# Kernel tuning notes

Hardware: AMD Instinct MI355X
Metric: run time of the kernel (lower is better)

Reference implementation:

```python
import jax, jax.numpy as jnp
import numpy as np

K_TOP = 32
TEMPERATURE = 0.1
EPS = 1e-12  # torch F.normalize eps


def _l2_normalize(x):
    n = jnp.linalg.norm(x, axis=-1, keepdims=True)
    return x / jnp.maximum(n, EPS)


def setup_inputs() -> dict:
    key = jax.random.key(0)
    kq, kk, kv = jax.random.split(key, 3)
    B, T, d_k, d_v, N = 4, 512, 512, 512, 65536
    queries = jax.random.normal(kq, (B, T, d_k), dtype=jnp.float32)
    keys = jax.random.normal(kk, (N, d_k), dtype=jnp.float32)
    values = jax.random.normal(kv, (N, d_v), dtype=jnp.float32)
    return {"queries": queries, "keys": keys, "values": values}


def reference(queries, keys, values):
    B, T, d_k = queries.shape
    d_v = values.shape[1]
    flat_q = queries.reshape(B * T, d_k)
    qn = _l2_normalize(flat_q)           # [BT, d_k]
    kn = _l2_normalize(keys)             # [N, d_k]
    scores = qn @ kn.T                   # [BT, N] cosine similarities
    topk_scores, topk_idx = jax.lax.top_k(scores, K_TOP)  # [BT, K]
    attn = jax.nn.softmax(topk_scores / TEMPERATURE, axis=-1)  # [BT, K]
    retrieved = values[topk_idx]         # [BT, K, d_v]
    aggregated = jnp.einsum('nk,nkd->nd', attn, retrieved)  # [BT, d_v]
    return (aggregated.reshape(B, T, d_v),
            attn.reshape(B, T, K_TOP),
            topk_idx.reshape(B, T, K_TOP))
```

## Files before the change

### kernel.cpp

```cpp
#include <hip/hip_runtime.h>
#include <math.h>

#define M_ROWS 2048
#define N_KEYS 65536
#define DKK 512
#define DVV 512
#define KTOP 32
#define NSPLIT 32
#define NRANGE (N_KEYS / NSPLIT)
#define BM 128
#define BN 128
#define NTILES (NRANGE / BN)
#define KSTEPS (DKK / 32)
#define CAP 8

typedef _Float16 f16x8 __attribute__((ext_vector_type(8)));
typedef _Float16 f16x4v __attribute__((ext_vector_type(4)));
typedef float f32x4 __attribute__((ext_vector_type(4)));


__device__ __forceinline__ void split4(const float4 v, float inv,
                                       _Float16* ph, _Float16* pl) {
  f16x4v h, l;
  float y;
  y = v.x * inv; h[0] = (_Float16)y; l[0] = (_Float16)(y - (float)h[0]);
  y = v.y * inv; h[1] = (_Float16)y; l[1] = (_Float16)(y - (float)h[1]);
  y = v.z * inv; h[2] = (_Float16)y; l[2] = (_Float16)(y - (float)h[2]);
  y = v.w * inv; h[3] = (_Float16)y; l[3] = (_Float16)(y - (float)h[3]);
  *(f16x4v*)ph = h; *(f16x4v*)pl = l;
}

__global__ void __launch_bounds__(256) norm_split_kernel(
    const float* __restrict__ q, const float* __restrict__ keys,
    _Float16* __restrict__ Qh, _Float16* __restrict__ Ql,
    _Float16* __restrict__ Kh, _Float16* __restrict__ Kl) {
  const int gw = (blockIdx.x * 256 + threadIdx.x) >> 6;
  const int lane = threadIdx.x & 63;
  const float* row; _Float16 *oh, *ol;
  if (gw < M_ROWS) {
    row = q + (size_t)gw * DKK; oh = Qh + (size_t)gw * DKK; ol = Ql + (size_t)gw * DKK;
  } else {
    const int n = gw - M_ROWS;
    if (n >= N_KEYS) return;
    row = keys + (size_t)n * DKK; oh = Kh + (size_t)n * DKK; ol = Kl + (size_t)n * DKK;
  }
  const float4 a = ((const float4*)row)[lane];
  const float4 b = ((const float4*)row)[lane + 64];
  float s = a.x*a.x + a.y*a.y + a.z*a.z + a.w*a.w
          + b.x*b.x + b.y*b.y + b.z*b.z + b.w*b.w;
#pragma unroll
  for (int off = 32; off; off >>= 1) s += __shfl_xor(s, off);
  const float inv = 1.0f / fmaxf(sqrtf(s), 1e-12f);
  split4(a, inv, oh + lane * 4,       ol + lane * 4);
  split4(b, inv, oh + 256 + lane * 4, ol + 256 + lane * 4);
}

__device__ __forceinline__ void insert32(float* tS, int* tI, float s, int idx) {
  const float ms = tS[31]; const int mi_ = tI[31];
  if (s < ms || (s == ms && idx > mi_)) return;
  int p = 0;
  while (p < KTOP && (tS[p] > s || (tS[p] == s && tI[p] < idx))) ++p;
  for (int qq = KTOP - 1; qq > p; --qq) { tS[qq] = tS[qq-1]; tI[qq] = tI[qq-1]; }
  tS[p] = s; tI[p] = idx;
}

__global__ void __launch_bounds__(256, 2) gemm_topk_kernel(
    const _Float16* __restrict__ Qh, const _Float16* __restrict__ Ql,
    const _Float16* __restrict__ Kh, const _Float16* __restrict__ Kl,
    float* __restrict__ pscore, int* __restrict__ pidx) {
  __shared__ _Float16 stAh[BM*32], stAl[BM*32], stBh[BN*32], stBl[BN*32];
  __shared__ float topS[128*33];
  __shared__ int   topI[128*33];
  __shared__ float candS[128*9];
  __shared__ int   candI[128*9];
  __shared__ float mS[128];
  __shared__ int   cnt[128];
  __shared__ int   sOver;

  const int tid  = threadIdx.x;
  const int lane = tid & 63;
  const int w    = tid >> 6;
  const int wr   = w >> 1, wc = w & 1;
  const int cl   = lane & 15;
  const int g    = lane >> 4;
  const int g4   = g * 4;
  const int qbase  = blockIdx.x * BM;
  const int nbase0 = blockIdx.y * NRANGE;

  if (tid < 128) {
    mS[tid] = -INFINITY; cnt[tid] = 0;
#pragma unroll
    for (int j = 0; j < KTOP; ++j) { topS[tid*33+j] = -INFINITY; topI[tid*33+j] = 0x7fffffff; }
  }
  if (tid == 0) sOver = 0;
  __syncthreads();

  for (int ct = 0; ct < NTILES; ++ct) {
    const int n0 = nbase0 + ct * BN;
    f32x4 acc[4][4];
#pragma unroll
    for (int mi = 0; mi < 4; ++mi)
#pragma unroll
      for (int ni = 0; ni < 4; ++ni) acc[mi][ni] = (f32x4)0.0f;

    for (int ks = 0; ks < KSTEPS; ++ks) {
      const int kof = ks * 32;
      f16x8 ld[8];
#pragma unroll
      for (int p = 0; p < 2; ++p) {
        const int id = tid + p * 256;
        const int r = id >> 2, o = id & 3;
        const size_t ga = (size_t)(qbase + r) * DKK + kof + o * 8;
        const size_t gb = (size_t)(n0 + r) * DKK + kof + o * 8;
        ld[p*4+0] = *(const f16x8*)&Qh[ga];
        ld[p*4+1] = *(const f16x8*)&Ql[ga];
        ld[p*4+2] = *(const f16x8*)&Kh[gb];
        ld[p*4+3] = *(const f16x8*)&Kl[gb];
      }
      __syncthreads();
#pragma unroll
      for (int p = 0; p < 2; ++p) {
        const int id = tid + p * 256;
        const int r = id >> 2, o = id & 3;
        const int sw = r * 32 + 8 * (o ^ ((r >> 1) & 3));
        *(f16x8*)&stAh[sw] = ld[p*4+0];
        *(f16x8*)&stAl[sw] = ld[p*4+1];
        *(f16x8*)&stBh[sw] = ld[p*4+2];
        *(f16x8*)&stBl[sw] = ld[p*4+3];
      }
      __syncthreads();

      f16x8 Ah[4], Al[4], Bh[4], Bl[4];
#pragma unroll
      for (int mi = 0; mi < 4; ++mi) {
        const int r = wr * 64 + mi * 16 + cl;
        const int sw = r * 32 + 8 * (g ^ ((r >> 1) & 3));
        Ah[mi] = *(const f16x8*)&stAh[sw];
        Al[mi] = *(const f16x8*)&stAl[sw];
      }
#pragma unroll
      for (int ni = 0; ni < 4; ++ni) {
        const int c = wc * 64 + ni * 16 + cl;
        const int sw = c * 32 + 8 * (g ^ ((c >> 1) & 3));
        Bh[ni] = *(const f16x8*)&stBh[sw];
        Bl[ni] = *(const f16x8*)&stBl[sw];
      }
#pragma unroll
      for (int mi = 0; mi < 4; ++mi)
#pragma unroll
        for (int ni = 0; ni < 4; ++ni) {
          acc[mi][ni] = __builtin_amdgcn_mfma_f32_16x16x32_f16(Al[mi], Bl[ni], acc[mi][ni], 0, 0, 0);
          acc[mi][ni] = __builtin_amdgcn_mfma_f32_16x16x32_f16(Al[mi], Bh[ni], acc[mi][ni], 0, 0, 0);
          acc[mi][ni] = __builtin_amdgcn_mfma_f32_16x16x32_f16(Ah[mi], Bl[ni], acc[mi][ni], 0, 0, 0);
          acc[mi][ni] = __builtin_amdgcn_mfma_f32_16x16x32_f16(Ah[mi], Bh[ni], acc[mi][ni], 0, 0, 0);
        }
    }

    float m[4][4];
#pragma unroll
    for (int mi = 0; mi < 4; ++mi) {
      const f32x4 mv = *(const f32x4*)&mS[wr * 64 + mi * 16 + g4];
      m[mi][0] = mv[0]; m[mi][1] = mv[1]; m[mi][2] = mv[2]; m[mi][3] = mv[3];
    }
    unsigned long long pend = 0ull;
#pragma unroll
    for (int mi = 0; mi < 4; ++mi)
#pragma unroll
      for (int ni = 0; ni < 4; ++ni)
#pragma unroll
        for (int j = 0; j < 4; ++j)
          if (acc[mi][ni][j] >= m[mi][j])
            pend |= 1ull << (mi * 16 + ni * 4 + j);

    for (;;) {
      if (pend) {
#pragma unroll
        for (int mi = 0; mi < 4; ++mi)
#pragma unroll
          for (int ni = 0; ni < 4; ++ni)
#pragma unroll
            for (int j = 0; j < 4; ++j) {
              const int bit = mi * 16 + ni * 4 + j;
              if (pend & (1ull << bit)) {
                const int r = wr * 64 + mi * 16 + g4 + j;
                const int t = atomicAdd(&cnt[r], 1);
                if (t < CAP) {
                  candS[r * 9 + t] = acc[mi][ni][j];
                  candI[r * 9 + t] = n0 + wc * 64 + ni * 16 + cl;
                  pend &= ~(1ull << bit);
                }
              }
            }
      }
      __syncthreads();
      if (tid < 128) {
        int nc = cnt[tid];
        if (nc > CAP) { sOver = 1; nc = CAP; }
        float* tS = &topS[tid * 33];
        int*   tI = &topI[tid * 33];
        for (int e = 0; e < nc; ++e) insert32(tS, tI, candS[tid * 9 + e], candI[tid * 9 + e]);
        mS[tid] = tS[KTOP - 1];
        cnt[tid] = 0;
      }
      __syncthreads();
      const int over = sOver;
      __syncthreads();
      if (tid == 0) sOver = 0;
      if (!over) break;
#pragma unroll
      for (int mi = 0; mi < 4; ++mi) {
        const f32x4 mv = *(const f32x4*)&mS[wr * 64 + mi * 16 + g4];
        m[mi][0] = mv[0]; m[mi][1] = mv[1]; m[mi][2] = mv[2]; m[mi][3] = mv[3];
      }
      unsigned long long keep = 0ull;
#pragma unroll
      for (int mi = 0; mi < 4; ++mi)
#pragma unroll
        for (int ni = 0; ni < 4; ++ni)
#pragma unroll
          for (int j = 0; j < 4; ++j) {
            const int bit = mi * 16 + ni * 4 + j;
            if ((pend & (1ull << bit)) && acc[mi][ni][j] >= m[mi][j])
              keep |= 1ull << bit;
          }
      pend = keep;
    }
  }

  if (tid < 128) {
    const size_t base = ((size_t)(qbase + tid) * NSPLIT + blockIdx.y) * KTOP;
    for (int j = 0; j < KTOP; ++j) {
      pscore[base + j] = topS[tid * 33 + j];
      pidx[base + j]   = topI[tid * 33 + j];
    }
  }
}


#define QB 128
#define NB 128
#define KC 32
#define FNTILES (NRANGE / NB)
#define KCH (DKK / KC)
#define LDST 132

__global__ void __launch_bounds__(256) norm_kernel(
    const float* __restrict__ q, const float* __restrict__ keys,
    float* __restrict__ qn, float* __restrict__ kinv) {
  const int gw = (blockIdx.x * 256 + threadIdx.x) >> 6;
  const int lane = threadIdx.x & 63;
  if (gw < M_ROWS) {
    const float* row = q + (size_t)gw * DKK;
    float4 a = ((const float4*)row)[lane];
    float4 b = ((const float4*)row)[lane + 64];
    float s = a.x*a.x + a.y*a.y + a.z*a.z + a.w*a.w
            + b.x*b.x + b.y*b.y + b.z*b.z + b.w*b.w;
#pragma unroll
    for (int off = 32; off; off >>= 1) s += __shfl_xor(s, off);
    const float inv = 1.0f / fmaxf(sqrtf(s), 1e-12f);
    float* orow = qn + (size_t)gw * DKK;
    ((float4*)orow)[lane]      = make_float4(a.x*inv, a.y*inv, a.z*inv, a.w*inv);
    ((float4*)orow)[lane + 64] = make_float4(b.x*inv, b.y*inv, b.z*inv, b.w*inv);
  } else {
    const int n = gw - M_ROWS;
    if (n < N_KEYS) {
      const float* row = keys + (size_t)n * DKK;
      float4 a = ((const float4*)row)[lane];
      float4 b = ((const float4*)row)[lane + 64];
      float s = a.x*a.x + a.y*a.y + a.z*a.z + a.w*a.w
              + b.x*b.x + b.y*b.y + b.z*b.z + b.w*b.w;
#pragma unroll
      for (int off = 32; off; off >>= 1) s += __shfl_xor(s, off);
      if (lane == 0) kinv[n] = 1.0f / fmaxf(sqrtf(s), 1e-12f);
    }
  }
}

__device__ __forceinline__ void lds_wr_tile(float* dst, int k8, int r, float4 v, float scale) {
  dst[(k8 * 4 + 0) * LDST + r] = v.x * scale;
  dst[(k8 * 4 + 1) * LDST + r] = v.y * scale;
  dst[(k8 * 4 + 2) * LDST + r] = v.z * scale;
  dst[(k8 * 4 + 3) * LDST + r] = v.w * scale;
}

__global__ void __launch_bounds__(256, 1) score_topk_kernel(
    const float* __restrict__ qn, const float* __restrict__ keys,
    const float* __restrict__ kinv,
    float* __restrict__ pscore, int* __restrict__ pidx) {
  __shared__ float u[16896];
  __shared__ float topS[QB * KTOP];
  __shared__ int   topI[QB * KTOP];

  const int tid = threadIdx.x;
  const int tx = tid & 15, ty = tid >> 4;
  const int qbase = blockIdx.y * QB;
  const int nbase0 = blockIdx.x * NRANGE;

  for (int i = tid; i < QB * KTOP; i += 256) { topS[i] = -INFINITY; topI[i] = 0; }
  __syncthreads();

  for (int t = 0; t < FNTILES; ++t) {
    const int n0 = nbase0 + t * NB;
    float acc[8][8];
#pragma unroll
    for (int i = 0; i < 8; ++i)
#pragma unroll
      for (int j = 0; j < 8; ++j) acc[i][j] = 0.0f;

#pragma unroll
    for (int p = 0; p < 4; ++p) {
      const int id = tid + p * 256;
      const int r = id >> 3, k8 = id & 7;
      const float4 va = *(const float4*)&qn[(size_t)(qbase + r) * DKK + k8 * 4];
      const float4 vb = *(const float4*)&keys[(size_t)(n0 + r) * DKK + k8 * 4];
      const float kv = kinv[n0 + r];
      lds_wr_tile(u, k8, r, va, 1.0f);
      lds_wr_tile(u + 4224, k8, r, vb, kv);
    }
    __syncthreads();

    for (int kc = 0; kc < KCH; ++kc) {
      float4 pa[4], pb[4]; float pk[4];
      const bool pre = (kc + 1 < KCH);
      if (pre) {
#pragma unroll
        for (int p = 0; p < 4; ++p) {
          const int id = tid + p * 256;
          const int r = id >> 3, k8 = id & 7;
          pa[p] = *(const float4*)&qn[(size_t)(qbase + r) * DKK + (kc + 1) * KC + k8 * 4];
          pb[p] = *(const float4*)&keys[(size_t)(n0 + r) * DKK + (kc + 1) * KC + k8 * 4];
          pk[p] = kinv[n0 + r];
        }
      }
      const float* As = u + (kc & 1) * 8448;
      const float* Bs = As + 4224;
#pragma unroll 4
      for (int kk = 0; kk < KC; ++kk) {
        const float4 a0 = *(const float4*)&As[kk * LDST + ty * 4];
        const float4 a1 = *(const float4*)&As[kk * LDST + ty * 4 + 64];
        const float4 b0 = *(const float4*)&Bs[kk * LDST + tx * 4];
        const float4 b1 = *(const float4*)&Bs[kk * LDST + tx * 4 + 64];
        const float av[8] = {a0.x,a0.y,a0.z,a0.w,a1.x,a1.y,a1.z,a1.w};
        const float bv[8] = {b0.x,b0.y,b0.z,b0.w,b1.x,b1.y,b1.z,b1.w};
#pragma unroll
        for (int i = 0; i < 8; ++i)
#pragma unroll
          for (int j = 0; j < 8; ++j)
            acc[i][j] = fmaf(av[i], bv[j], acc[i][j]);
      }
      if (pre) {
        float* Ad = u + ((kc + 1) & 1) * 8448;
        float* Bd = Ad + 4224;
#pragma unroll
        for (int p = 0; p < 4; ++p) {
          const int id = tid + p * 256;
          const int r = id >> 3, k8 = id & 7;
          lds_wr_tile(Ad, k8, r, pa[p], 1.0f);
          lds_wr_tile(Bd, k8, r, pb[p], pk[p]);
        }
      }
      __syncthreads();
    }

#pragma unroll
    for (int ib = 0; ib < 2; ++ib)
#pragma unroll
      for (int i = 0; i < 4; ++i) {
        const int r = ty * 4 + i + ib * 64;
#pragma unroll
        for (int jb = 0; jb < 2; ++jb) {
          *(float4*)&u[r * LDST + tx * 4 + jb * 64] =
              make_float4(acc[ib*4+i][jb*4+0], acc[ib*4+i][jb*4+1],
                          acc[ib*4+i][jb*4+2], acc[ib*4+i][jb*4+3]);
        }
      }
    __syncthreads();

    if (tid < QB) {
      const int row = tid;
      float* tS = &topS[row * KTOP];
      int*   tI = &topI[row * KTOP];
      float mSv = tS[KTOP - 1]; int mIv = tI[KTOP - 1];
      for (int c4 = 0; c4 < NB / 4; ++c4) {
        const float4 v = *(const float4*)&u[row * LDST + c4 * 4];
#pragma unroll
        for (int wv = 0; wv < 4; ++wv) {
          const float s = (&v.x)[wv];
          const int idx = n0 + c4 * 4 + wv;
          if (s > mSv || (s == mSv && idx < mIv)) {
            int p = 0;
            while (p < KTOP && (tS[p] > s || (tS[p] == s && tI[p] < idx))) ++p;
            for (int qq = KTOP - 1; qq > p; --qq) { tS[qq] = tS[qq-1]; tI[qq] = tI[qq-1]; }
            tS[p] = s; tI[p] = idx;
            mSv = tS[KTOP - 1]; mIv = tI[KTOP - 1];
          }
        }
      }
    }
    __syncthreads();
  }

  if (tid < QB) {
    const size_t base = ((size_t)(qbase + tid) * NSPLIT + blockIdx.x) * KTOP;
    for (int j = 0; j < KTOP; ++j) {
      pscore[base + j] = topS[tid * KTOP + j];
      pidx[base + j]   = topI[tid * KTOP + j];
    }
  }
}

__global__ void __launch_bounds__(256) merge_kernel(
    const float* __restrict__ pscore, const int* __restrict__ pidx,
    const float* __restrict__ values,
    float* __restrict__ out_agg, float* __restrict__ out_attn, float* __restrict__ out_idx) {
  __shared__ float attn_s[KTOP];
  __shared__ int   sel_i[KTOP];
  const int row = blockIdx.x;
  const int tid = threadIdx.x;

  if (tid < 64) {
    const int lane = tid;
    const float* ps = pscore + (size_t)row * NSPLIT * KTOP;
    const int*   pi = pidx   + (size_t)row * NSPLIT * KTOP;
    int pos = 0;
    float s; int idx;
    if (lane < NSPLIT) { s = ps[lane * KTOP]; idx = pi[lane * KTOP]; }
    else { s = -INFINITY; idx = 0x7fffffff; }
    for (int it = 0; it < KTOP; ++it) {
      float wsv = s; int wi = idx; int wl = lane;
#pragma unroll
      for (int off = 32; off; off >>= 1) {
        const float os = __shfl_xor(wsv, off);
        const int   oi = __shfl_xor(wi, off);
        const int   ol = __shfl_xor(wl, off);
        if (os > wsv || (os == wsv && oi < wi)) { wsv = os; wi = oi; wl = ol; }
      }
      if (lane == 0) { attn_s[it] = wsv; sel_i[it] = wi; }
      if (lane == wl) {
        ++pos;
        if (pos < KTOP) { s = ps[lane * KTOP + pos]; idx = pi[lane * KTOP + pos]; }
        else { s = -INFINITY; idx = 0x7fffffff; }
      }
    }
  }
  __syncthreads();
  if (tid < KTOP) {
    const float mm = attn_s[0];
    const float e = expf((attn_s[tid] - mm) * 10.0f);
    float tsum = e;
#pragma unroll
    for (int off = 16; off; off >>= 1) tsum += __shfl_xor(tsum, off);
    const float a = e / tsum;
    out_attn[(size_t)row * KTOP + tid] = a;
    out_idx [(size_t)row * KTOP + tid] = (float)sel_i[tid];
    attn_s[tid] = a;
  }
  __syncthreads();

  const int d = tid * 2;
  float2 accv = make_float2(0.0f, 0.0f);
  for (int j = 0; j < KTOP; ++j) {
    const float wgt = attn_s[j];
    const float2 v = *(const float2*)&values[(size_t)sel_i[j] * DVV + d];
    accv.x = fmaf(wgt, v.x, accv.x);
    accv.y = fmaf(wgt, v.y, accv.y);
  }
  *(float2*)&out_agg[(size_t)row * DVV + d] = accv;
}

extern "C" void kernel_launch(void* const* d_in, const int* in_sizes, int n_in,
                              void* d_out, int out_size, void* d_ws, size_t ws_size,
                              hipStream_t stream) {
  const float* q      = (const float*)d_in[0];
  const float* keys   = (const float*)d_in[1];
  const float* values = (const float*)d_in[2];

  float* out      = (float*)d_out;
  float* out_agg  = out;
  float* out_attn = out + (size_t)M_ROWS * DVV;
  float* out_idx  = out_attn + (size_t)M_ROWS * KTOP;

  const size_t needFast =
      (size_t)M_ROWS * DKK * 2 * 2
    + (size_t)N_KEYS * DKK * 2 * 2
    + (size_t)M_ROWS * NSPLIT * KTOP * 8;

  if (ws_size >= needFast) {
    _Float16* Qh = (_Float16*)d_ws;
    _Float16* Ql = Qh + (size_t)M_ROWS * DKK;
    _Float16* Kh = Ql + (size_t)M_ROWS * DKK;
    _Float16* Kl = Kh + (size_t)N_KEYS * DKK;
    float* pscore = (float*)(Kl + (size_t)N_KEYS * DKK);
    int*   pidx   = (int*)(pscore + (size_t)M_ROWS * NSPLIT * KTOP);

    norm_split_kernel<<<(M_ROWS + N_KEYS) / 4, 256, 0, stream>>>(q, keys, Qh, Ql, Kh, Kl);
    dim3 g2(M_ROWS / BM, NSPLIT, 1);
    gemm_topk_kernel<<<g2, 256, 0, stream>>>(Qh, Ql, Kh, Kl, pscore, pidx);
    merge_kernel<<<M_ROWS, 256, 0, stream>>>(pscore, pidx, values, out_agg, out_attn, out_idx);
  } else {
    float* ws     = (float*)d_ws;
    float* qn     = ws;
    float* kinv   = qn + (size_t)M_ROWS * DKK;
    float* pscore = kinv + N_KEYS;
    int*   pidx   = (int*)(pscore + (size_t)M_ROWS * NSPLIT * KTOP);

    norm_kernel<<<(M_ROWS + N_KEYS) / 4, 256, 0, stream>>>(q, keys, qn, kinv);
    dim3 g2(NSPLIT, M_ROWS / QB, 1);
    score_topk_kernel<<<g2, 256, 0, stream>>>(qn, keys, kinv, pscore, pidx);
    merge_kernel<<<M_ROWS, 256, 0, stream>>>(pscore, pidx, values, out_agg, out_attn, out_idx);
  }
}
```

Measured before the change: 1.569 ms.

## Prefetch next k-step into registers, drop low*low MFMA, swizzle block order

Loads for the next k-step (or the first step of the next tile) now go into a second register buffer, so global loads overlap with the MFMAs of the current step. The low*low MFMA term of the split-fp16 product is removed, leaving three MFMAs per tile pair instead of four. Blocks are also remapped so that consecutive launches spread across key splits, which changes L2 reuse, and shared-memory swizzle offsets are computed once up front. Costs are more registers for the double buffer at 2 blocks per SM and a small precision loss that could change top-k order on near-ties.

```diff
diff --git a/kernel.cpp b/kernel.cpp
--- a/kernel.cpp
+++ b/kernel.cpp
@@ -64,11 +64,28 @@
   tS[p] = s; tI[p] = idx;
 }
 
+#define LOADREGS(B, NN, KOF) do {                                        \
+  const size_t _q0 = qa0 + (size_t)(KOF), _q1 = qa1 + (size_t)(KOF);     \
+  const size_t _k0 = (size_t)(NN) * DKK + ka0 + (size_t)(KOF);           \
+  const size_t _k1 = (size_t)(NN) * DKK + ka1 + (size_t)(KOF);           \
+  B[0] = *(const f16x8*)&Qh[_q0]; B[1] = *(const f16x8*)&Ql[_q0];        \
+  B[2] = *(const f16x8*)&Kh[_k0]; B[3] = *(const f16x8*)&Kl[_k0];        \
+  B[4] = *(const f16x8*)&Qh[_q1]; B[5] = *(const f16x8*)&Ql[_q1];        \
+  B[6] = *(const f16x8*)&Kh[_k1]; B[7] = *(const f16x8*)&Kl[_k1];        \
+} while (0)
+
+#define WRITELDS(B) do {                                                 \
+  *(f16x8*)&stAh[sw0] = B[0]; *(f16x8*)&stAl[sw0] = B[1];                \
+  *(f16x8*)&stBh[sw0] = B[2]; *(f16x8*)&stBl[sw0] = B[3];                \
+  *(f16x8*)&stAh[sw1] = B[4]; *(f16x8*)&stAl[sw1] = B[5];                \
+  *(f16x8*)&stBh[sw1] = B[6]; *(f16x8*)&stBl[sw1] = B[7];                \
+} while (0)
+
 __global__ void __launch_bounds__(256, 2) gemm_topk_kernel(
     const _Float16* __restrict__ Qh, const _Float16* __restrict__ Ql,
     const _Float16* __restrict__ Kh, const _Float16* __restrict__ Kl,
     float* __restrict__ pscore, int* __restrict__ pidx) {
-  __shared__ _Float16 stAh[BM*32], stAl[BM*32], stBh[BN*32], stBl[BN*32];
+  __shared__ __attribute__((aligned(16))) _Float16 stAh[BM*32], stAl[BM*32], stBh[BN*32], stBl[BN*32];
   __shared__ float topS[128*33];
   __shared__ int   topI[128*33];
   __shared__ float candS[128*9];
@@ -84,8 +101,34 @@
   const int cl   = lane & 15;
   const int g    = lane >> 4;
   const int g4   = g * 4;
-  const int qbase  = blockIdx.x * BM;
-  const int nbase0 = blockIdx.y * NRANGE;
+
+  const int lin   = (int)(blockIdx.x + gridDim.x * blockIdx.y);
+  const int virt  = (lin & 7) * 64 + (lin >> 3);
+  const int mblk  = virt & 15;
+  const int split = virt >> 4;
+  const int qbase  = mblk * BM;
+  const int nbase0 = split * NRANGE;
+
+  const int r0 = tid >> 2, o0 = tid & 3;
+  const int r1 = r0 + 64;
+  const size_t qa0 = (size_t)(qbase + r0) * DKK + o0 * 8;
+  const size_t qa1 = qa0 + (size_t)64 * DKK;
+  const size_t ka0 = (size_t)r0 * DKK + o0 * 8;
+  const size_t ka1 = ka0 + (size_t)64 * DKK;
+  const int sw0 = r0 * 32 + 8 * (o0 ^ ((r0 >> 1) & 3));
+  const int sw1 = r1 * 32 + 8 * (o0 ^ ((r1 >> 1) & 3));
+
+  int swA[4], swB[4];
+#pragma unroll
+  for (int mi = 0; mi < 4; ++mi) {
+    const int r = wr * 64 + mi * 16 + cl;
+    swA[mi] = r * 32 + 8 * (g ^ ((r >> 1) & 3));
+  }
+#pragma unroll
+  for (int ni = 0; ni < 4; ++ni) {
+    const int c = wc * 64 + ni * 16 + cl;
+    swB[ni] = c * 32 + 8 * (g ^ ((c >> 1) & 3));
+  }
 
   if (tid < 128) {
     mS[tid] = -INFINITY; cnt[tid] = 0;
@@ -94,6 +137,9 @@
   }
   if (tid == 0) sOver = 0;
   __syncthreads();
+
+  f16x8 bufA[8], bufB[8];
+  LOADREGS(bufA, nbase0, 0);
 
   for (int ct = 0; ct < NTILES; ++ct) {
     const int n0 = nbase0 + ct * BN;
@@ -103,53 +149,34 @@
 #pragma unroll
       for (int ni = 0; ni < 4; ++ni) acc[mi][ni] = (f32x4)0.0f;
 
+#pragma unroll
     for (int ks = 0; ks < KSTEPS; ++ks) {
-      const int kof = ks * 32;
-      f16x8 ld[8];
-#pragma unroll
-      for (int p = 0; p < 2; ++p) {
-        const int id = tid + p * 256;
-        const int r = id >> 2, o = id & 3;
-        const size_t ga = (size_t)(qbase + r) * DKK + kof + o * 8;
-        const size_t gb = (size_t)(n0 + r) * DKK + kof + o * 8;
-        ld[p*4+0] = *(const f16x8*)&Qh[ga];
-        ld[p*4+1] = *(const f16x8*)&Ql[ga];
-        ld[p*4+2] = *(const f16x8*)&Kh[gb];
-        ld[p*4+3] = *(const f16x8*)&Kl[gb];
-      }
       __syncthreads();
-#pragma unroll
-      for (int p = 0; p < 2; ++p) {
-        const int id = tid + p * 256;
-        const int r = id >> 2, o = id & 3;
-        const int sw = r * 32 + 8 * (o ^ ((r >> 1) & 3));
-        *(f16x8*)&stAh[sw] = ld[p*4+0];
-        *(f16x8*)&stAl[sw] = ld[p*4+1];
-        *(f16x8*)&stBh[sw] = ld[p*4+2];
-        *(f16x8*)&stBl[sw] = ld[p*4+3];
-      }
+      if ((ks & 1) == 0) WRITELDS(bufA); else WRITELDS(bufB);
       __syncthreads();
 
+      if (ks < KSTEPS - 1) {
+        if ((ks & 1) == 0) { LOADREGS(bufB, n0, (ks + 1) * 32); }
+        else               { LOADREGS(bufA, n0, (ks + 1) * 32); }
+      } else if (ct + 1 < NTILES) {
+        LOADREGS(bufA, n0 + BN, 0);
+      }
+
       f16x8 Ah[4], Al[4], Bh[4], Bl[4];
 #pragma unroll
       for (int mi = 0; mi < 4; ++mi) {
-        const int r = wr * 64 + mi * 16 + cl;
-        const int sw = r * 32 + 8 * (g ^ ((r >> 1) & 3));
-        Ah[mi] = *(const f16x8*)&stAh[sw];
-        Al[mi] = *(const f16x8*)&stAl[sw];
+        Ah[mi] = *(const f16x8*)&stAh[swA[mi]];
+        Al[mi] = *(const f16x8*)&stAl[swA[mi]];
       }
 #pragma unroll
       for (int ni = 0; ni < 4; ++ni) {
-        const int c = wc * 64 + ni * 16 + cl;
-        const int sw = c * 32 + 8 * (g ^ ((c >> 1) & 3));
-        Bh[ni] = *(const f16x8*)&stBh[sw];
-        Bl[ni] = *(const f16x8*)&stBl[sw];
+        Bh[ni] = *(const f16x8*)&stBh[swB[ni]];
+        Bl[ni] = *(const f16x8*)&stBl[swB[ni]];
       }
 #pragma unroll
       for (int mi = 0; mi < 4; ++mi)
 #pragma unroll
         for (int ni = 0; ni < 4; ++ni) {
-          acc[mi][ni] = __builtin_amdgcn_mfma_f32_16x16x32_f16(Al[mi], Bl[ni], acc[mi][ni], 0, 0, 0);
           acc[mi][ni] = __builtin_amdgcn_mfma_f32_16x16x32_f16(Al[mi], Bh[ni], acc[mi][ni], 0, 0, 0);
           acc[mi][ni] = __builtin_amdgcn_mfma_f32_16x16x32_f16(Ah[mi], Bl[ni], acc[mi][ni], 0, 0, 0);
           acc[mi][ni] = __builtin_amdgcn_mfma_f32_16x16x32_f16(Ah[mi], Bh[ni], acc[mi][ni], 0, 0, 0);
@@ -228,7 +255,7 @@
   }
 
   if (tid < 128) {
-    const size_t base = ((size_t)(qbase + tid) * NSPLIT + blockIdx.y) * KTOP;
+    const size_t base = ((size_t)(qbase + tid) * NSPLIT + split) * KTOP;
     for (int j = 0; j < KTOP; ++j) {
       pscore[base + j] = topS[tid * 33 + j];
       pidx[base + j]   = topI[tid * 33 + j];
```

New measurement: 1.865 ms. 1.19x slower.

## Double-buffer GEMM tiles via direct global-to-LDS loads, halve BM, drop lo*lo MFMA

Applied to the files above, without the earlier changes.

Rewrites the GEMM+top-k kernel to stage tiles with global_load_lds into double-buffered LDS, prefetching the next k-step while computing the current one, so each k-step needs one barrier instead of two. It halves the query tile to 64 rows, which doubles the grid, remaps block IDs for XCD/L2 locality, and raises the candidate cap. It also drops the Al*Bl MFMA term of the split-fp16 product, cutting matrix work by a quarter at a small precision cost that could affect top-k ordering near ties.

```diff
diff --git a/kernel.cpp b/kernel.cpp
--- a/kernel.cpp
+++ b/kernel.cpp
@@ -8,11 +8,13 @@
 #define KTOP 32
 #define NSPLIT 32
 #define NRANGE (N_KEYS / NSPLIT)
-#define BM 128
+#define BM 64
 #define BN 128
+#define MBLKS (M_ROWS / BM)
 #define NTILES (NRANGE / BN)
 #define KSTEPS (DKK / 32)
-#define CAP 8
+#define CAP 12
+#define CSTR 13
 
 typedef _Float16 f16x8 __attribute__((ext_vector_type(8)));
 typedef _Float16 f16x4v __attribute__((ext_vector_type(4)));
@@ -64,17 +66,36 @@
   tS[p] = s; tI[p] = idx;
 }
 
+#define STAGE(BUF, N0, KS) do {                                                \
+  const size_t _ko = (size_t)(KS) * 32;                                        \
+  const size_t _qa = qsrc + _ko;                                               \
+  const size_t _ba = (size_t)(N0) * DKK + bsrc + _ko;                          \
+  __builtin_amdgcn_global_load_lds((const __attribute__((address_space(1))) void*)(Qh + _qa), \
+      (__attribute__((address_space(3))) void*)&stA[BUF][0][ldsA], 16, 0, 0);  \
+  __builtin_amdgcn_global_load_lds((const __attribute__((address_space(1))) void*)(Ql + _qa), \
+      (__attribute__((address_space(3))) void*)&stA[BUF][1][ldsA], 16, 0, 0);  \
+  __builtin_amdgcn_global_load_lds((const __attribute__((address_space(1))) void*)(Kh + _ba), \
+      (__attribute__((address_space(3))) void*)&stB[BUF][0][ldsA], 16, 0, 0);  \
+  __builtin_amdgcn_global_load_lds((const __attribute__((address_space(1))) void*)(Kh + _ba + 64 * DKK), \
+      (__attribute__((address_space(3))) void*)&stB[BUF][0][2048 + ldsA], 16, 0, 0); \
+  __builtin_amdgcn_global_load_lds((const __attribute__((address_space(1))) void*)(Kl + _ba), \
+      (__attribute__((address_space(3))) void*)&stB[BUF][1][ldsA], 16, 0, 0);  \
+  __builtin_amdgcn_global_load_lds((const __attribute__((address_space(1))) void*)(Kl + _ba + 64 * DKK), \
+      (__attribute__((address_space(3))) void*)&stB[BUF][1][2048 + ldsA], 16, 0, 0); \
+} while (0)
+
 __global__ void __launch_bounds__(256, 2) gemm_topk_kernel(
     const _Float16* __restrict__ Qh, const _Float16* __restrict__ Ql,
     const _Float16* __restrict__ Kh, const _Float16* __restrict__ Kl,
     float* __restrict__ pscore, int* __restrict__ pidx) {
-  __shared__ _Float16 stAh[BM*32], stAl[BM*32], stBh[BN*32], stBl[BN*32];
-  __shared__ float topS[128*33];
-  __shared__ int   topI[128*33];
-  __shared__ float candS[128*9];
-  __shared__ int   candI[128*9];
-  __shared__ float mS[128];
-  __shared__ int   cnt[128];
+  __shared__ __attribute__((aligned(16))) _Float16 stA[2][2][BM * 32];
+  __shared__ __attribute__((aligned(16))) _Float16 stB[2][2][BN * 32];
+  __shared__ float topS[BM * 33];
+  __shared__ int   topI[BM * 33];
+  __shared__ float candS[BM * CSTR];
+  __shared__ int   candI[BM * CSTR];
+  __shared__ float mS[BM];
+  __shared__ int   cnt[BM];
   __shared__ int   sOver;
 
   const int tid  = threadIdx.x;
@@ -84,121 +105,120 @@
   const int cl   = lane & 15;
   const int g    = lane >> 4;
   const int g4   = g * 4;
-  const int qbase  = blockIdx.x * BM;
-  const int nbase0 = blockIdx.y * NRANGE;
-
-  if (tid < 128) {
+
+  const int lin   = (int)(blockIdx.x + gridDim.x * blockIdx.y);
+  const int virt  = (lin & 7) * 128 + (lin >> 3);
+  const int mblk  = virt & (MBLKS - 1);
+  const int split = virt >> 5;
+  const int qbase  = mblk * BM;
+  const int nbase0 = split * NRANGE;
+
+  const int soct = (tid & 3) ^ ((tid >> 3) & 3);
+  const int ldsA = tid * 8;
+  const size_t qsrc = (size_t)(qbase + (tid >> 2)) * DKK + (size_t)soct * 8;
+  const size_t bsrc = (size_t)(tid >> 2) * DKK + (size_t)soct * 8;
+
+  int offA[2], offB[4];
+#pragma unroll
+  for (int mi = 0; mi < 2; ++mi) {
+    const int r = wr * 32 + mi * 16 + cl;
+    offA[mi] = r * 32 + (g ^ ((r >> 1) & 3)) * 8;
+  }
+#pragma unroll
+  for (int ni = 0; ni < 4; ++ni) {
+    const int c = wc * 64 + ni * 16 + cl;
+    offB[ni] = c * 32 + (g ^ ((c >> 1) & 3)) * 8;
+  }
+
+  if (tid < BM) {
     mS[tid] = -INFINITY; cnt[tid] = 0;
 #pragma unroll
     for (int j = 0; j < KTOP; ++j) { topS[tid*33+j] = -INFINITY; topI[tid*33+j] = 0x7fffffff; }
   }
   if (tid == 0) sOver = 0;
+
+  STAGE(0, nbase0, 0);
   __syncthreads();
 
   for (int ct = 0; ct < NTILES; ++ct) {
     const int n0 = nbase0 + ct * BN;
-    f32x4 acc[4][4];
-#pragma unroll
-    for (int mi = 0; mi < 4; ++mi)
+    f32x4 acc[2][4];
+#pragma unroll
+    for (int mi = 0; mi < 2; ++mi)
 #pragma unroll
       for (int ni = 0; ni < 4; ++ni) acc[mi][ni] = (f32x4)0.0f;
 
+#pragma unroll 2
     for (int ks = 0; ks < KSTEPS; ++ks) {
-      const int kof = ks * 32;
-      f16x8 ld[8];
-#pragma unroll
-      for (int p = 0; p < 2; ++p) {
-        const int id = tid + p * 256;
-        const int r = id >> 2, o = id & 3;
-        const size_t ga = (size_t)(qbase + r) * DKK + kof + o * 8;
-        const size_t gb = (size_t)(n0 + r) * DKK + kof + o * 8;
-        ld[p*4+0] = *(const f16x8*)&Qh[ga];
-        ld[p*4+1] = *(const f16x8*)&Ql[ga];
-        ld[p*4+2] = *(const f16x8*)&Kh[gb];
-        ld[p*4+3] = *(const f16x8*)&Kl[gb];
-      }
-      __syncthreads();
-#pragma unroll
-      for (int p = 0; p < 2; ++p) {
-        const int id = tid + p * 256;
-        const int r = id >> 2, o = id & 3;
-        const int sw = r * 32 + 8 * (o ^ ((r >> 1) & 3));
-        *(f16x8*)&stAh[sw] = ld[p*4+0];
-        *(f16x8*)&stAl[sw] = ld[p*4+1];
-        *(f16x8*)&stBh[sw] = ld[p*4+2];
-        *(f16x8*)&stBl[sw] = ld[p*4+3];
-      }
-      __syncthreads();
-
-      f16x8 Ah[4], Al[4], Bh[4], Bl[4];
-#pragma unroll
-      for (int mi = 0; mi < 4; ++mi) {
-        const int r = wr * 64 + mi * 16 + cl;
-        const int sw = r * 32 + 8 * (g ^ ((r >> 1) & 3));
-        Ah[mi] = *(const f16x8*)&stAh[sw];
-        Al[mi] = *(const f16x8*)&stAl[sw];
+      const int cur = ks & 1;
+      if (ks < KSTEPS - 1)        { STAGE(cur ^ 1, n0, ks + 1); }
+      else if (ct + 1 < NTILES)   { STAGE(cur ^ 1, n0 + BN, 0); }
+
+      f16x8 Ah[2], Al[2], Bh[4], Bl[4];
+#pragma unroll
+      for (int mi = 0; mi < 2; ++mi) {
+        Ah[mi] = *(const f16x8*)&stA[cur][0][offA[mi]];
+        Al[mi] = *(const f16x8*)&stA[cur][1][offA[mi]];
       }
 #pragma unroll
       for (int ni = 0; ni < 4; ++ni) {
-        const int c = wc * 64 + ni * 16 + cl;
-        const int sw = c * 32 + 8 * (g ^ ((c >> 1) & 3));
-        Bh[ni] = *(const f16x8*)&stBh[sw];
-        Bl[ni] = *(const f16x8*)&stBl[sw];
-      }
-#pragma unroll
-      for (int mi = 0; mi < 4; ++mi)
+        Bh[ni] = *(const f16x8*)&stB[cur][0][offB[ni]];
+        Bl[ni] = *(const f16x8*)&stB[cur][1][offB[ni]];
+      }
+#pragma unroll
+      for (int mi = 0; mi < 2; ++mi)
 #pragma unroll
         for (int ni = 0; ni < 4; ++ni) {
-          acc[mi][ni] = __builtin_amdgcn_mfma_f32_16x16x32_f16(Al[mi], Bl[ni], acc[mi][ni], 0, 0, 0);
           acc[mi][ni] = __builtin_amdgcn_mfma_f32_16x16x32_f16(Al[mi], Bh[ni], acc[mi][ni], 0, 0, 0);
           acc[mi][ni] = __builtin_amdgcn_mfma_f32_16x16x32_f16(Ah[mi], Bl[ni], acc[mi][ni], 0, 0, 0);
           acc[mi][ni] = __builtin_amdgcn_mfma_f32_16x16x32_f16(Ah[mi], Bh[ni], acc[mi][ni], 0, 0, 0);
         }
-    }
-
-    float m[4][4];
-#pragma unroll
-    for (int mi = 0; mi < 4; ++mi) {
-      const f32x4 mv = *(const f32x4*)&mS[wr * 64 + mi * 16 + g4];
+      __syncthreads();
+    }
+
+    float m[2][4];
+#pragma unroll
+    for (int mi = 0; mi < 2; ++mi) {
+      const f32x4 mv = *(const f32x4*)&mS[wr * 32 + mi * 16 + g4];
       m[mi][0] = mv[0]; m[mi][1] = mv[1]; m[mi][2] = mv[2]; m[mi][3] = mv[3];
     }
-    unsigned long long pend = 0ull;
-#pragma unroll
-    for (int mi = 0; mi < 4; ++mi)
+    unsigned int pend = 0u;
+#pragma unroll
+    for (int mi = 0; mi < 2; ++mi)
 #pragma unroll
       for (int ni = 0; ni < 4; ++ni)
 #pragma unroll
         for (int j = 0; j < 4; ++j)
           if (acc[mi][ni][j] >= m[mi][j])
-            pend |= 1ull << (mi * 16 + ni * 4 + j);
+            pend |= 1u << (mi * 16 + ni * 4 + j);
 
     for (;;) {
       if (pend) {
 #pragma unroll
-        for (int mi = 0; mi < 4; ++mi)
+        for (int mi = 0; mi < 2; ++mi)
 #pragma unroll
           for (int ni = 0; ni < 4; ++ni)
 #pragma unroll
             for (int j = 0; j < 4; ++j) {
               const int bit = mi * 16 + ni * 4 + j;
-              if (pend & (1ull << bit)) {
-                const int r = wr * 64 + mi * 16 + g4 + j;
+              if (pend & (1u << bit)) {
+                const int r = wr * 32 + mi * 16 + g4 + j;
                 const int t = atomicAdd(&cnt[r], 1);
                 if (t < CAP) {
-                  candS[r * 9 + t] = acc[mi][ni][j];
-                  candI[r * 9 + t] = n0 + wc * 64 + ni * 16 + cl;
-                  pend &= ~(1ull << bit);
+                  candS[r * CSTR + t] = acc[mi][ni][j];
+                  candI[r * CSTR + t] = n0 + wc * 64 + ni * 16 + cl;
+                  pend &= ~(1u << bit);
                 }
               }
             }
       }
       __syncthreads();
-      if (tid < 128) {
+      if (tid < BM) {
         int nc = cnt[tid];
         if (nc > CAP) { sOver = 1; nc = CAP; }
         float* tS = &topS[tid * 33];
         int*   tI = &topI[tid * 33];
-        for (int e = 0; e < nc; ++e) insert32(tS, tI, candS[tid * 9 + e], candI[tid * 9 + e]);
+        for (int e = 0; e < nc; ++e) insert32(tS, tI, candS[tid * CSTR + e], candI[tid * CSTR + e]);
         mS[tid] = tS[KTOP - 1];
         cnt[tid] = 0;
       }
@@ -208,27 +228,27 @@
       if (tid == 0) sOver = 0;
       if (!over) break;
 #pragma unroll
-      for (int mi = 0; mi < 4; ++mi) {
-        const f32x4 mv = *(const f32x4*)&mS[wr * 64 + mi * 16 + g4];
+      for (int mi = 0; mi < 2; ++mi) {
+        const f32x4 mv = *(const f32x4*)&mS[wr * 32 + mi * 16 + g4];
         m[mi][0] = mv[0]; m[mi][1] = mv[1]; m[mi][2] = mv[2]; m[mi][3] = mv[3];
       }
-      unsigned long long keep = 0ull;
-#pragma unroll
-      for (int mi = 0; mi < 4; ++mi)
+      unsigned int keep = 0u;
+#pragma unroll
+      for (int mi = 0; mi < 2; ++mi)
 #pragma unroll
         for (int ni = 0; ni < 4; ++ni)
 #pragma unroll
           for (int j = 0; j < 4; ++j) {
             const int bit = mi * 16 + ni * 4 + j;
-            if ((pend & (1ull << bit)) && acc[mi][ni][j] >= m[mi][j])
-              keep |= 1ull << bit;
+            if ((pend & (1u << bit)) && acc[mi][ni][j] >= m[mi][j])
+              keep |= 1u << bit;
           }
       pend = keep;
     }
   }
 
-  if (tid < 128) {
-    const size_t base = ((size_t)(qbase + tid) * NSPLIT + blockIdx.y) * KTOP;
+  if (tid < BM) {
+    const size_t base = ((size_t)(qbase + tid) * NSPLIT + split) * KTOP;
     for (int j = 0; j < KTOP; ++j) {
       pscore[base + j] = topS[tid * 33 + j];
       pidx[base + j]   = topI[tid * 33 + j];
@@ -494,7 +514,7 @@
     int*   pidx   = (int*)(pscore + (size_t)M_ROWS * NSPLIT * KTOP);
 
     norm_split_kernel<<<(M_ROWS + N_KEYS) / 4, 256, 0, stream>>>(q, keys, Qh, Ql, Kh, Kl);
-    dim3 g2(M_ROWS / BM, NSPLIT, 1);
+    dim3 g2(MBLKS, NSPLIT, 1);
     gemm_topk_kernel<<<g2, 256, 0, stream>>>(Qh, Ql, Kh, Kl, pscore, pidx);
     merge_kernel<<<M_ROWS, 256, 0, stream>>>(pscore, pidx, values, out_agg, out_attn, out_idx);
   } else {
```

Result: slower. 2.371 ms (+51.1%).
